# Optimization experiments

Measured on AMD Instinct MI355X. Metric: run time of the kernel, lower is better.

Reference implementation:

```python
import jax, jax.numpy as jnp
import numpy as np

H = 2048  # hidden_size
B = 16    # batch
S = 2048  # source (values) length
T = 16    # decoder state length per layer
L = 1     # num_layers


def setup_inputs() -> dict:
    key = jax.random.key(0)
    ks = jax.random.split(key, 6)
    sc = 1.0 / np.sqrt(H)
    return {
        "query": jax.random.normal(ks[0], (L, B, T, H), dtype=jnp.float32),
        "values": jax.random.normal(ks[1], (B, S, H), dtype=jnp.float32),
        "mask": jnp.ones((B, S), dtype=jnp.bool_),  # unused by the module
        "W1_w": jax.random.normal(ks[2], (H, H), dtype=jnp.float32) * sc,
        "W1_b": jnp.zeros((H,), dtype=jnp.float32),
        "W2_w": jax.random.normal(ks[3], (H, H), dtype=jnp.float32) * sc,
        "W2_b": jnp.zeros((H,), dtype=jnp.float32),
        "V_w": jax.random.normal(ks[4], (H,), dtype=jnp.float32) * sc,
        "V_b": jnp.zeros((), dtype=jnp.float32),
    }


def reference(query, values, mask, W1_w, W1_b, W2_w, W2_b, V_w, V_b):
    # query: (L,B,T,H); non-bidirectional path keeps last time step of layer 0
    q = query[0][:, -1:, :]                        # (B,1,H)
    q_proj = q @ W1_w.T + W1_b                     # (B,1,H)
    # Faithful quirk of the source: W2 is applied to values[0] (batch elem 0)
    v_proj = values[0] @ W2_w.T + W2_b             # (S,H)
    # broadcast add -> (B,S,H), tanh, project with V -> (B,S)
    scores = jnp.tanh(q_proj + v_proj[None, :, :]) @ V_w + V_b  # (B,S)
    scores = scores[:, None, :]                    # (B,1,S)
    alphas = jax.nn.softmax(scores, axis=-1)       # (B,1,S)
    context = jnp.einsum('bqs,bsh->bqh', alphas, values)  # (B,1,H)
    return context, alphas
```

## Files before the change

kernel.cpp:

```cpp
#include <hip/hip_runtime.h>
#include <stdint.h>

#define H 2048
#define B 16
#define S 2048
#define SCH 32
#define SPC (S / SCH)

typedef __attribute__((ext_vector_type(4))) float f32x4;
typedef __attribute__((ext_vector_type(8))) __bf16 bf16x8;
typedef __attribute__((ext_vector_type(4))) short s16x4;

__device__ inline unsigned short f2bf(float f) {
    uint32_t u = __builtin_bit_cast(uint32_t, f);
    uint32_t r = (u + 0x7FFFu + ((u >> 16) & 1u)) >> 16;
    return (unsigned short)r;
}

__device__ inline void global_load_lds16(const unsigned short* g, unsigned short* l) {
    __builtin_amdgcn_global_load_lds(
        (const __attribute__((address_space(1))) void*)g,
        (__attribute__((address_space(3))) void*)l, 16, 0, 0);
}

__global__ __launch_bounds__(256) void convert2_kernel(
    const float* __restrict__ v0, const float* __restrict__ w2,
    unsigned short* __restrict__ Vb, unsigned short* __restrict__ W2b)
{
    const int n4 = (S * H) / 4;
    int i = blockIdx.x * blockDim.x + threadIdx.x;
    int stride = gridDim.x * blockDim.x;
    for (; i < 2 * n4; i += stride) {
        const float* src = (i < n4) ? v0 : w2;
        unsigned short* dst = (i < n4) ? Vb : W2b;
        int j = (i < n4) ? i : i - n4;
        f32x4 v = ((const f32x4*)src)[j];
        s16x4 o;
        #pragma unroll
        for (int k = 0; k < 4; ++k) o[k] = (short)f2bf(v[k]);
        ((s16x4*)dst)[j] = o;
    }
}

__global__ __launch_bounds__(256) void qproj_kernel(
    const float* __restrict__ query,
    const float* __restrict__ w1,
    const float* __restrict__ w1b,
    const float* __restrict__ w2b,
    float* __restrict__ qproj)
{
    int wid = threadIdx.x >> 6;
    int lane = threadIdx.x & 63;
    int h = blockIdx.x * 4 + wid;
    float acc[B];
    #pragma unroll
    for (int b = 0; b < B; ++b) acc[b] = 0.f;
    const float* wrow = w1 + (int64_t)h * H;
    for (int kc = 0; kc < H; kc += 256) {
        f32x4 w4 = *(const f32x4*)(wrow + kc + lane * 4);
        #pragma unroll
        for (int b = 0; b < B; ++b) {
            const float* q = query + ((int64_t)(b * 16 + 15)) * H + kc + lane * 4;
            f32x4 q4 = *(const f32x4*)q;
            acc[b] += w4.x * q4.x + w4.y * q4.y + w4.z * q4.z + w4.w * q4.w;
        }
    }
    #pragma unroll
    for (int b = 0; b < B; ++b) {
        float v = acc[b];
        #pragma unroll
        for (int off = 32; off > 0; off >>= 1) v += __shfl_down(v, off, 64);
        if (lane == 0) qproj[b * H + h] = v + w1b[h] + w2b[h];
    }
}

#define GM 64
#define GN 128
#define GK 32
#define NT (H / GK)

__global__ __launch_bounds__(256) void gemm_bt_kernel(
    const unsigned short* __restrict__ A,
    const unsigned short* __restrict__ Bm,
    float* __restrict__ C)
{
    __shared__ unsigned short smA[3][GM * GK];
    __shared__ unsigned short smB[3][GN * GK];

    int t = threadIdx.x;
    int lane = t & 63;
    int wid = t >> 6;
    int wr = wid >> 1, wc = wid & 1;
    int brow = blockIdx.y * GM;
    int bcol = blockIdx.x * GN;
    int l15 = lane & 15;
    int lk = (lane >> 4) * 8;

    f32x4 acc[2][4] = {};

    const unsigned short* gA = A + (int64_t)(brow + (t >> 2)) * H + (t & 3) * 8;
    const unsigned short* gB = Bm + (int64_t)(bcol + (t >> 2)) * H + (t & 3) * 8;

    unsigned short* pA0 = smA[0]; unsigned short* pB0 = smB[0];
    unsigned short* pA1 = smA[1]; unsigned short* pB1 = smB[1];
    unsigned short* pA2 = smA[2]; unsigned short* pB2 = smB[2];

    global_load_lds16(gA, pA0 + t * 8);
    global_load_lds16(gB, pB0 + t * 8);
    global_load_lds16(gB + 64 * H, pB0 + (t + 256) * 8);
    global_load_lds16(gA + GK, pA1 + t * 8);
    global_load_lds16(gB + GK, pB1 + t * 8);
    global_load_lds16(gB + 64 * H + GK, pB1 + (t + 256) * 8);
    asm volatile("s_waitcnt vmcnt(3)" ::: "memory");
    __builtin_amdgcn_s_barrier();
    __builtin_amdgcn_sched_barrier(0);

    for (int kt = 0; kt < NT; ++kt) {
        int kn = (kt + 2) * GK;
        if (kn < H) {
            global_load_lds16(gA + kn, pA2 + t * 8);
            global_load_lds16(gB + kn, pB2 + t * 8);
            global_load_lds16(gB + 64 * H + kn, pB2 + (t + 256) * 8);
        }
        bf16x8 a[2], b[4];
        #pragma unroll
        for (int m = 0; m < 2; ++m)
            a[m] = *(const bf16x8*)&pA0[(wr * 32 + m * 16 + l15) * GK + lk];
        #pragma unroll
        for (int n = 0; n < 4; ++n)
            b[n] = *(const bf16x8*)&pB0[(wc * 64 + n * 16 + l15) * GK + lk];
        #pragma unroll
        for (int m = 0; m < 2; ++m)
            #pragma unroll
            for (int n = 0; n < 4; ++n)
                acc[m][n] = __builtin_amdgcn_mfma_f32_16x16x32_bf16(a[m], b[n], acc[m][n], 0, 0, 0);
        if (kn < H) asm volatile("s_waitcnt vmcnt(3)" ::: "memory");
        else        asm volatile("s_waitcnt vmcnt(0)" ::: "memory");
        __builtin_amdgcn_s_barrier();
        __builtin_amdgcn_sched_barrier(0);
        unsigned short* tmp;
        tmp = pA0; pA0 = pA1; pA1 = pA2; pA2 = tmp;
        tmp = pB0; pB0 = pB1; pB1 = pB2; pB2 = tmp;
    }

    #pragma unroll
    for (int m = 0; m < 2; ++m) {
        #pragma unroll
        for (int n = 0; n < 4; ++n) {
            int col = bcol + wc * 64 + n * 16 + l15;
            #pragma unroll
            for (int q = 0; q < 4; ++q) {
                int row = brow + wr * 32 + m * 16 + (lane >> 4) * 4 + q;
                C[(int64_t)row * H + col] = acc[m][n][q];
            }
        }
    }
}

#define K2LOG2E 2.8853900817779268f

__global__ __launch_bounds__(256) void scores_kernel(
    const float* __restrict__ vproj,
    const float* __restrict__ qproj,
    const float* __restrict__ vw,
    float* __restrict__ scores)
{
    int wid = threadIdx.x >> 6, lane = threadIdx.x & 63;
    int s = blockIdx.x * 4 + wid;
    float acc[B];
    #pragma unroll
    for (int b = 0; b < B; ++b) acc[b] = 0.f;
    const float* vrow = vproj + (int64_t)s * H;
    for (int hc = 0; hc < H; hc += 256) {
        f32x4 vp = *(const f32x4*)(vrow + hc + lane * 4);
        f32x4 w4 = *(const f32x4*)(vw + hc + lane * 4);
        #pragma unroll
        for (int b = 0; b < B; ++b) {
            f32x4 q4 = *(const f32x4*)(qproj + b * H + hc + lane * 4);
            #pragma unroll
            for (int j = 0; j < 4; ++j) {
                float x = q4[j] + vp[j];
                float e = __builtin_amdgcn_exp2f(x * K2LOG2E);
                float r = __builtin_amdgcn_rcpf(e + 1.0f);
                acc[b] = fmaf(w4[j], r, acc[b]);
            }
        }
    }
    #pragma unroll
    for (int b = 0; b < B; ++b) {
        float v = acc[b];
        #pragma unroll
        for (int off = 32; off > 0; off >>= 1) v += __shfl_down(v, off, 64);
        if (lane == 0) scores[b * S + s] = -2.0f * v;
    }
}

__global__ __launch_bounds__(256) void softmax_kernel(
    const float* __restrict__ scores,
    float* __restrict__ alphas)
{
    __shared__ float red[8];
    int b = blockIdx.x;
    int t = threadIdx.x;
    int wid = t >> 6, lane = t & 63;
    const float* srow = scores + b * S;
    float v[8];
    float m = -1e30f;
    #pragma unroll
    for (int i = 0; i < 8; ++i) { v[i] = srow[t + i * 256]; m = fmaxf(m, v[i]); }
    #pragma unroll
    for (int off = 32; off > 0; off >>= 1) m = fmaxf(m, __shfl_xor(m, off, 64));
    if (lane == 0) red[wid] = m;
    __syncthreads();
    m = fmaxf(fmaxf(red[0], red[1]), fmaxf(red[2], red[3]));
    float sum = 0.f;
    #pragma unroll
    for (int i = 0; i < 8; ++i) { v[i] = __expf(v[i] - m); sum += v[i]; }
    #pragma unroll
    for (int off = 32; off > 0; off >>= 1) sum += __shfl_xor(sum, off, 64);
    if (lane == 0) red[4 + wid] = sum;
    __syncthreads();
    sum = red[4] + red[5] + red[6] + red[7];
    float inv = 1.f / sum;
    #pragma unroll
    for (int i = 0; i < 8; ++i) alphas[b * S + t + i * 256] = v[i] * inv;
}

__global__ __launch_bounds__(256) void context_partial_kernel(
    const float* __restrict__ values,
    const float* __restrict__ alphas,
    float* __restrict__ partial)
{
    int ht = blockIdx.x;
    int sc = blockIdx.y;
    int b  = blockIdx.z;
    int h = ht * 1024 + threadIdx.x * 4;
    const float* vbase = values + (int64_t)b * S * H + (int64_t)sc * SPC * H + h;
    const float* abase = alphas + b * S + sc * SPC;
    f32x4 acc0 = {}, acc1 = {};
    #pragma unroll 4
    for (int s = 0; s < SPC; s += 2) {
        float a0 = abase[s], a1 = abase[s + 1];
        f32x4 v0 = *(const f32x4*)(vbase + (int64_t)s * H);
        f32x4 v1 = *(const f32x4*)(vbase + (int64_t)(s + 1) * H);
        acc0 += a0 * v0;
        acc1 += a1 * v1;
    }
    *(f32x4*)(partial + ((int64_t)(sc * B + b)) * H + h) = acc0 + acc1;
}

__global__ __launch_bounds__(256) void context_reduce_kernel(
    const float* __restrict__ partial, float* __restrict__ out)
{
    int idx = blockIdx.x * 256 + threadIdx.x;
    int b = idx >> 11, h = idx & 2047;
    float s = 0.f;
    #pragma unroll
    for (int c = 0; c < SCH; ++c) s += partial[((int64_t)(c * B + b)) * H + h];
    out[idx] = s;
}

extern "C" void kernel_launch(void* const* d_in, const int* in_sizes, int n_in,
                              void* d_out, int out_size, void* d_ws, size_t ws_size,
                              hipStream_t stream) {
    const float* query  = (const float*)d_in[0];
    const float* values = (const float*)d_in[1];
    const float* w1w = (const float*)d_in[3];
    const float* w1b = (const float*)d_in[4];
    const float* w2w = (const float*)d_in[5];
    const float* w2b = (const float*)d_in[6];
    const float* vw  = (const float*)d_in[7];

    float* out = (float*)d_out;
    float* context = out;
    float* alphas  = out + B * H;

    float* ws = (float*)d_ws;
    float* qproj   = ws;
    float* scores  = ws + 32768;
    float* vproj   = ws + 65536;
    float* partial = vproj + (int64_t)S * H;
    unsigned short* Vb  = (unsigned short*)(partial + SCH * B * H);
    unsigned short* W2b = Vb + S * H;

    convert2_kernel<<<2048, 256, 0, stream>>>(values, w2w, Vb, W2b);
    qproj_kernel<<<H / 4, 256, 0, stream>>>(query, w1w, w1b, w2b, qproj);
    gemm_bt_kernel<<<dim3(H / GN, S / GM), 256, 0, stream>>>(Vb, W2b, vproj);
    scores_kernel<<<S / 4, 256, 0, stream>>>(vproj, qproj, vw, scores);
    softmax_kernel<<<B, 256, 0, stream>>>(scores, alphas);
    context_partial_kernel<<<dim3(2, SCH, B), 256, 0, stream>>>(values, alphas, partial);
    context_reduce_kernel<<<(B * H) / 256, 256, 0, stream>>>(partial, context);
}
```

Before: 146.1 us.

## Double GEMM K-tile with XOR-swizzled LDS, fuse softmax into context kernel

The bf16 GEMM now stages a 64-wide K tile per pipeline stage and XOR-swizzles the LDS layout, with matching swizzled fragment reads, to avoid bank conflicts and halve the number of barrier iterations. Separately, the standalone softmax kernel is removed. Each context-partial block recomputes the row max and sum from the scores, normalizes its own chunk of alphas into LDS, and one block per chunk writes the alphas out. This removes a launch and a global round trip for alphas, but every block redundantly reduces a full score row and LDS use per GEMM block grows.

After: 133.1 us. 1.1x faster.

```diff
diff --git a/kernel.cpp b/kernel.cpp
--- a/kernel.cpp
+++ b/kernel.cpp
@@ -76,7 +76,7 @@
 
 #define GM 64
 #define GN 128
-#define GK 32
+#define GK 64
 #define NT (H / GK)
 
 __global__ __launch_bounds__(256) void gemm_bt_kernel(
@@ -94,47 +94,55 @@
     int brow = blockIdx.y * GM;
     int bcol = blockIdx.x * GN;
     int l15 = lane & 15;
-    int lk = (lane >> 4) * 8;
 
     f32x4 acc[2][4] = {};
 
-    const unsigned short* gA = A + (int64_t)(brow + (t >> 2)) * H + (t & 3) * 8;
-    const unsigned short* gB = Bm + (int64_t)(bcol + (t >> 2)) * H + (t & 3) * 8;
+    int srow = t >> 3;
+    int kslot = (t & 7) ^ (srow & 7);
+    const unsigned short* gA = A + (int64_t)(brow + srow) * H + kslot * 8;
+    const unsigned short* gB = Bm + (int64_t)(bcol + srow) * H + kslot * 8;
 
     unsigned short* pA0 = smA[0]; unsigned short* pB0 = smB[0];
     unsigned short* pA1 = smA[1]; unsigned short* pB1 = smB[1];
     unsigned short* pA2 = smA[2]; unsigned short* pB2 = smB[2];
 
-    global_load_lds16(gA, pA0 + t * 8);
-    global_load_lds16(gB, pB0 + t * 8);
-    global_load_lds16(gB + 64 * H, pB0 + (t + 256) * 8);
-    global_load_lds16(gA + GK, pA1 + t * 8);
-    global_load_lds16(gB + GK, pB1 + t * 8);
-    global_load_lds16(gB + 64 * H + GK, pB1 + (t + 256) * 8);
-    asm volatile("s_waitcnt vmcnt(3)" ::: "memory");
+#define STAGE(pa, pb, koff) do {                                        \
+        global_load_lds16(gA + (koff), (pa) + t * 8);                   \
+        global_load_lds16(gA + 32 * H + (koff), (pa) + (t + 256) * 8);  \
+        global_load_lds16(gB + (koff), (pb) + t * 8);                   \
+        global_load_lds16(gB + 32 * H + (koff), (pb) + (t + 256) * 8);  \
+        global_load_lds16(gB + 64 * H + (koff), (pb) + (t + 512) * 8);  \
+        global_load_lds16(gB + 96 * H + (koff), (pb) + (t + 768) * 8);  \
+    } while (0)
+
+    int swz = (((lane >> 4) ^ (lane & 7)) << 3);
+
+    STAGE(pA0, pB0, 0);
+    STAGE(pA1, pB1, GK);
+    asm volatile("s_waitcnt vmcnt(6)" ::: "memory");
     __builtin_amdgcn_s_barrier();
     __builtin_amdgcn_sched_barrier(0);
 
     for (int kt = 0; kt < NT; ++kt) {
         int kn = (kt + 2) * GK;
-        if (kn < H) {
-            global_load_lds16(gA + kn, pA2 + t * 8);
-            global_load_lds16(gB + kn, pB2 + t * 8);
-            global_load_lds16(gB + 64 * H + kn, pB2 + (t + 256) * 8);
+        if (kn < H) STAGE(pA2, pB2, kn);
+        #pragma unroll
+        for (int kk = 0; kk < 2; ++kk) {
+            int sw = swz ^ (kk << 5);
+            bf16x8 a[2], b[4];
+            #pragma unroll
+            for (int m = 0; m < 2; ++m)
+                a[m] = *(const bf16x8*)&pA0[(wr * 32 + m * 16 + l15) * GK + sw];
+            #pragma unroll
+            for (int n = 0; n < 4; ++n)
+                b[n] = *(const bf16x8*)&pB0[(wc * 64 + n * 16 + l15) * GK + sw];
+            #pragma unroll
+            for (int m = 0; m < 2; ++m)
+                #pragma unroll
+                for (int n = 0; n < 4; ++n)
+                    acc[m][n] = __builtin_amdgcn_mfma_f32_16x16x32_bf16(a[m], b[n], acc[m][n], 0, 0, 0);
         }
-        bf16x8 a[2], b[4];
-        #pragma unroll
-        for (int m = 0; m < 2; ++m)
-            a[m] = *(const bf16x8*)&pA0[(wr * 32 + m * 16 + l15) * GK + lk];
-        #pragma unroll
-        for (int n = 0; n < 4; ++n)
-            b[n] = *(const bf16x8*)&pB0[(wc * 64 + n * 16 + l15) * GK + lk];
-        #pragma unroll
-        for (int m = 0; m < 2; ++m)
-            #pragma unroll
-            for (int n = 0; n < 4; ++n)
-                acc[m][n] = __builtin_amdgcn_mfma_f32_16x16x32_bf16(a[m], b[n], acc[m][n], 0, 0, 0);
-        if (kn < H) asm volatile("s_waitcnt vmcnt(3)" ::: "memory");
+        if (kn < H) asm volatile("s_waitcnt vmcnt(6)" ::: "memory");
         else        asm volatile("s_waitcnt vmcnt(0)" ::: "memory");
         __builtin_amdgcn_s_barrier();
         __builtin_amdgcn_sched_barrier(0);
@@ -142,6 +150,7 @@
         tmp = pA0; pA0 = pA1; pA1 = pA2; pA2 = tmp;
         tmp = pB0; pB0 = pB1; pB1 = pB2; pB2 = tmp;
     }
+#undef STAGE
 
     #pragma unroll
     for (int m = 0; m < 2; ++m) {
@@ -195,14 +204,19 @@
     }
 }
 
-__global__ __launch_bounds__(256) void softmax_kernel(
+__global__ __launch_bounds__(256) void context_partial_kernel(
+    const float* __restrict__ values,
     const float* __restrict__ scores,
-    float* __restrict__ alphas)
+    float* __restrict__ alphas,
+    float* __restrict__ partial)
 {
     __shared__ float red[8];
-    int b = blockIdx.x;
-    int t = threadIdx.x;
-    int wid = t >> 6, lane = t & 63;
+    __shared__ float a_lds[SPC];
+    int ht = blockIdx.x;
+    int sc = blockIdx.y;
+    int b  = blockIdx.z;
+    int t = threadIdx.x, wid = t >> 6, lane = t & 63;
+
     const float* srow = scores + b * S;
     float v[8];
     float m = -1e30f;
@@ -215,32 +229,26 @@
     m = fmaxf(fmaxf(red[0], red[1]), fmaxf(red[2], red[3]));
     float sum = 0.f;
     #pragma unroll
-    for (int i = 0; i < 8; ++i) { v[i] = __expf(v[i] - m); sum += v[i]; }
+    for (int i = 0; i < 8; ++i) sum += __expf(v[i] - m);
     #pragma unroll
     for (int off = 32; off > 0; off >>= 1) sum += __shfl_xor(sum, off, 64);
     if (lane == 0) red[4 + wid] = sum;
     __syncthreads();
-    sum = red[4] + red[5] + red[6] + red[7];
-    float inv = 1.f / sum;
-    #pragma unroll
-    for (int i = 0; i < 8; ++i) alphas[b * S + t + i * 256] = v[i] * inv;
-}
-
-__global__ __launch_bounds__(256) void context_partial_kernel(
-    const float* __restrict__ values,
-    const float* __restrict__ alphas,
-    float* __restrict__ partial)
-{
-    int ht = blockIdx.x;
-    int sc = blockIdx.y;
-    int b  = blockIdx.z;
-    int h = ht * 1024 + threadIdx.x * 4;
+    float inv = 1.f / (red[4] + red[5] + red[6] + red[7]);
+
+    if (t < SPC) {
+        float a = __expf(srow[sc * SPC + t] - m) * inv;
+        a_lds[t] = a;
+        if (ht == 0) alphas[b * S + sc * SPC + t] = a;
+    }
+    __syncthreads();
+
+    int h = ht * 1024 + t * 4;
     const float* vbase = values + (int64_t)b * S * H + (int64_t)sc * SPC * H + h;
-    const float* abase = alphas + b * S + sc * SPC;
     f32x4 acc0 = {}, acc1 = {};
     #pragma unroll 4
     for (int s = 0; s < SPC; s += 2) {
-        float a0 = abase[s], a1 = abase[s + 1];
+        float a0 = a_lds[s], a1 = a_lds[s + 1];
         f32x4 v0 = *(const f32x4*)(vbase + (int64_t)s * H);
         f32x4 v1 = *(const f32x4*)(vbase + (int64_t)(s + 1) * H);
         acc0 += a0 * v0;
@@ -287,7 +295,6 @@
     qproj_kernel<<<H / 4, 256, 0, stream>>>(query, w1w, w1b, w2b, qproj);
     gemm_bt_kernel<<<dim3(H / GN, S / GM), 256, 0, stream>>>(Vb, W2b, vproj);
     scores_kernel<<<S / 4, 256, 0, stream>>>(vproj, qproj, vw, scores);
-    softmax_kernel<<<B, 256, 0, stream>>>(scores, alphas);
-    context_partial_kernel<<<dim3(2, SCH, B), 256, 0, stream>>>(values, alphas, partial);
+    context_partial_kernel<<<dim3(2, SCH, B), 256, 0, stream>>>(values, scores, alphas, partial);
     context_reduce_kernel<<<(B * H) / 256, 256, 0, stream>>>(partial, context);
 }
```
